# Performance work log

Hardware: AMD Instinct MI355X
Metric: run time of the kernel (lower is better)

Reference implementation:

```python
import jax, jax.numpy as jnp
import numpy as np
from jax import lax
from functools import partial

NPOINT = 2048
RADIUS = 1.0
NSAMPLE = 32


def _fps(xyz, npoint):
    # Farthest point sampling, sequential as in the classic CUDA kernel.
    # xyz: (N, 3) -> (npoint,) int32 indices; starts at index 0.
    N = xyz.shape[0]
    init_d = jnp.full((N,), jnp.inf, dtype=xyz.dtype)

    def step(carry, _):
        dists, last = carry
        delta = xyz - xyz[last]                      # (N, 3)
        nd = jnp.sum(delta * delta, axis=-1)         # (N,)
        dists = jnp.minimum(dists, nd)
        nxt = jnp.argmax(dists).astype(jnp.int32)
        return (dists, nxt), last

    (_, _), idxs = lax.scan(step, (init_d, jnp.int32(0)), None, length=npoint)
    return idxs


def _ball_query(radius, nsample, xyz, new_xyz):
    # xyz: (N, 3), new_xyz: (S, 3) -> (S, nsample) int32.
    # Take the first nsample points (in original order) within radius of each
    # centroid; pad with the first found index (centroid itself always hits).
    N = xyz.shape[0]
    d2 = (jnp.sum(new_xyz * new_xyz, -1, keepdims=True)
          + jnp.sum(xyz * xyz, -1)[None, :]
          - 2.0 * new_xyz @ xyz.T)                   # (S, N)
    mask = d2 < radius * radius
    key = jnp.where(mask, jnp.arange(N, dtype=jnp.int32), jnp.int32(N))  # (S, N)
    neg_topk, _ = lax.top_k(-key, nsample)           # nsample smallest keys
    idx = -neg_topk                                  # (S, nsample), ascending
    first = idx[:, :1]
    return jnp.where(idx == N, first, idx)


def setup_inputs() -> dict:
    key = jax.random.key(0)
    inputs = jax.random.normal(key, (4, 8192, 16), dtype=jnp.float32)
    return {"inputs": inputs}


def reference(inputs):
    xyz = inputs[..., :3]                            # (B, N, 3)
    points = inputs[..., 3:]                         # (B, N, C)

    fps_idx = jax.vmap(lambda p: _fps(p, NPOINT))(xyz)          # (B, S)
    new_xyz = jnp.take_along_axis(xyz, fps_idx[..., None], axis=1)  # (B, S, 3)

    idx = jax.vmap(partial(_ball_query, RADIUS, NSAMPLE))(xyz, new_xyz)  # (B, S, K)

    gather = jax.vmap(lambda p, i: p[i])             # (N, C), (S, K) -> (S, K, C)
    grouped_xyz = gather(xyz, idx) - new_xyz[:, :, None, :]      # (B, S, K, 3)
    grouped_points = gather(points, idx)                         # (B, S, K, C)
    new_points = jnp.concatenate([grouped_xyz, grouped_points], axis=-1)
    return new_xyz, new_points, idx, grouped_xyz
```

## Files before the change

### kernel.cpp

```cpp
#include <hip/hip_runtime.h>

#define NPOINT 2048
#define NSAMPLE 32
#define NPTS 8192
#define NB 4
#define CH 16
#define FPS_THREADS 1024
#define PTS_PER_THREAD (NPTS / FPS_THREADS)
#define FPS_WAVES (FPS_THREADS / 64)

typedef unsigned long long u64;

#define OFF_NEWXYZ 0
#define OFF_NEWPTS (NB * NPOINT * 3)
#define OFF_IDX (OFF_NEWPTS + NB * NPOINT * NSAMPLE * CH)
#define OFF_GXYZ (OFF_IDX + NB * NPOINT * NSAMPLE)

template <int CTRL>
__device__ __forceinline__ u64 dpp_max_round(u64 key) {
  unsigned lo = (unsigned)key, hi = (unsigned)(key >> 32);
  unsigned plo =
      (unsigned)__builtin_amdgcn_update_dpp(0, (int)lo, CTRL, 0xf, 0xf, true);
  unsigned phi =
      (unsigned)__builtin_amdgcn_update_dpp(0, (int)hi, CTRL, 0xf, 0xf, true);
  u64 other = ((u64)phi << 32) | plo;
  return other > key ? other : key;
}

__global__ __launch_bounds__(FPS_THREADS) void fps_kernel(
    const float* __restrict__ in, float* __restrict__ out) {
  __shared__ float4 lpxyz[NPTS];
  __shared__ float newb[NPOINT * 3];
  __shared__ u64 slots[2][FPS_WAVES];

  const int b = blockIdx.x;
  const int tid = threadIdx.x;
  const int lane = tid & 63;
  const int wv = tid >> 6;
  const float* base = in + (size_t)b * NPTS * CH;

  float px[PTS_PER_THREAD], py[PTS_PER_THREAD], pz[PTS_PER_THREAD],
      d[PTS_PER_THREAD];
#pragma unroll
  for (int j = 0; j < PTS_PER_THREAD; ++j) {
    int p = tid + j * FPS_THREADS;
    float4 r = *reinterpret_cast<const float4*>(base + (size_t)p * CH);
    px[j] = r.x;
    py[j] = r.y;
    pz[j] = r.z;
    lpxyz[p] = r;
    d[j] = __builtin_inff();
  }
  if (tid < FPS_WAVES)
    slots[0][tid] = (tid == 0) ? (((u64)0x7f800000u << 32) | 8191u) : 0ull;

  for (int it = 0; it < NPOINT; ++it) {
    const int pb = it & 1;
    __syncthreads();
    u64 k = slots[pb][lane & 15];
    k = dpp_max_round<0x111>(k);
    k = dpp_max_round<0x112>(k);
    k = dpp_max_round<0x114>(k);
    k = dpp_max_round<0x118>(k);
    const int gi =
        8191 -
        (int)(unsigned)__builtin_amdgcn_readlane((int)(unsigned)k, 15);
    float4 g = lpxyz[gi];
    const float gx = g.x, gy = g.y, gz = g.z;
    if (tid == 0) {
      newb[it * 3 + 0] = gx;
      newb[it * 3 + 1] = gy;
      newb[it * 3 + 2] = gz;
    }
    float bestv = -1.0f;
    int bestj = 0;
#pragma unroll
    for (int j = 0; j < PTS_PER_THREAD; ++j) {
      float dx = __fsub_rn(px[j], gx);
      float dy = __fsub_rn(py[j], gy);
      float dz = __fsub_rn(pz[j], gz);
      float nd = __fadd_rn(__fadd_rn(__fmul_rn(dx, dx), __fmul_rn(dy, dy)),
                           __fmul_rn(dz, dz));
      float dn = fminf(d[j], nd);
      d[j] = dn;
      if (dn > bestv) {
        bestv = dn;
        bestj = j;
      }
    }
    const int besti = tid + bestj * FPS_THREADS;
    u64 bestkey = ((u64)__float_as_uint(bestv) << 32) | (8191u - (unsigned)besti);
    bestkey = dpp_max_round<0x111>(bestkey);
    bestkey = dpp_max_round<0x112>(bestkey);
    bestkey = dpp_max_round<0x114>(bestkey);
    bestkey = dpp_max_round<0x118>(bestkey);
    bestkey = dpp_max_round<0x142>(bestkey);
    bestkey = dpp_max_round<0x143>(bestkey);
    if (lane == 63) slots[pb ^ 1][wv] = bestkey;
  }
  __syncthreads();
  float* ob = out + OFF_NEWXYZ + (size_t)b * NPOINT * 3;
  for (int i = tid; i < NPOINT * 3; i += FPS_THREADS) ob[i] = newb[i];
}

__device__ __forceinline__ void write_slot(float* __restrict__ out,
                                           const float* __restrict__ base,
                                           int b, int qi, int s, int p,
                                           float4 r0, float qx, float qy,
                                           float qz) {
  float dx = __fsub_rn(r0.x, qx);
  float dy = __fsub_rn(r0.y, qy);
  float dz = __fsub_rn(r0.z, qz);
  size_t qs = (size_t)b * NPOINT + qi;
  out[OFF_IDX + qs * NSAMPLE + s] = (float)p;
  float* g = out + OFF_GXYZ + (qs * NSAMPLE + s) * 3;
  g[0] = dx;
  g[1] = dy;
  g[2] = dz;
  const float* row = base + (size_t)p * CH;
  float4 r1 = *reinterpret_cast<const float4*>(row + 4);
  float4 r2 = *reinterpret_cast<const float4*>(row + 8);
  float4 r3 = *reinterpret_cast<const float4*>(row + 12);
  float* np_ = out + OFF_NEWPTS + (qs * NSAMPLE + s) * CH;
  *reinterpret_cast<float4*>(np_ + 0) = make_float4(dx, dy, dz, r0.w);
  *reinterpret_cast<float4*>(np_ + 4) = r1;
  *reinterpret_cast<float4*>(np_ + 8) = r2;
  *reinterpret_cast<float4*>(np_ + 12) = r3;
}

__global__ __launch_bounds__(256) void ballq_kernel(
    const float* __restrict__ in, float* __restrict__ out) {
  const int lane = threadIdx.x & 63;
  const int qid = blockIdx.x * 4 + (threadIdx.x >> 6);
  const int b = qid >> 11;
  const int qi = qid & 2047;
  const float* base = in + (size_t)b * NPTS * CH;
  const float* q = out + OFF_NEWXYZ + ((size_t)b * NPOINT + qi) * 3;
  float qx = q[0], qy = q[1], qz = q[2];
  float qn = __fadd_rn(__fadd_rn(__fmul_rn(qx, qx), __fmul_rn(qy, qy)),
                       __fmul_rn(qz, qz));

  int cnt = 0;
  int first = 0;
  bool have_first = false;
  for (int chunk = 0; chunk < NPTS / 64 && cnt < NSAMPLE; ++chunk) {
    int p = chunk * 64 + lane;
    float4 r0 = *reinterpret_cast<const float4*>(base + (size_t)p * CH);
    float pn =
        __fadd_rn(__fadd_rn(__fmul_rn(r0.x, r0.x), __fmul_rn(r0.y, r0.y)),
                  __fmul_rn(r0.z, r0.z));
    float dot =
        __fadd_rn(__fadd_rn(__fmul_rn(qx, r0.x), __fmul_rn(qy, r0.y)),
                  __fmul_rn(qz, r0.z));
    float d2 = __fsub_rn(__fadd_rn(qn, pn), __fmul_rn(2.0f, dot));
    bool in_r = d2 < 1.0f;
    unsigned long long mask = __ballot(in_r);
    if (!have_first && mask) {
      first = chunk * 64 + __builtin_ctzll(mask);
      have_first = true;
    }
    int pos = cnt + __popcll(mask & ((1ull << lane) - 1ull));
    if (in_r && pos < NSAMPLE) write_slot(out, base, b, qi, pos, p, r0, qx, qy, qz);
    cnt += __popcll(mask);
  }
  if (cnt < NSAMPLE) {
    int s = cnt + lane;
    if (s < NSAMPLE) {
      float4 r0 = *reinterpret_cast<const float4*>(base + (size_t)first * CH);
      write_slot(out, base, b, qi, s, first, r0, qx, qy, qz);
    }
  }
}

extern "C" void kernel_launch(void* const* d_in, const int* in_sizes, int n_in,
                              void* d_out, int out_size, void* d_ws,
                              size_t ws_size, hipStream_t stream) {
  (void)in_sizes;
  (void)n_in;
  (void)out_size;
  (void)d_ws;
  (void)ws_size;
  const float* in = (const float*)d_in[0];
  float* out = (float*)d_out;
  fps_kernel<<<NB, FPS_THREADS, 0, stream>>>(in, out);
  ballq_kernel<<<(NB * NPOINT) / 4, 256, 0, stream>>>(in, out);
}
```

Measured before the change: 2.167 ms.

## Use float-only DPP max with ballot tie-break and packed v2f FPS math

The FPS argmax reduction used to run DPP max rounds on packed 64-bit (distance, index) keys. It now reduces only the 32-bit float distance with DPP, then finds the winning lane with a ballot and readlane. This roughly halves the DPP traffic per round. Points are now assigned to threads contiguously, so each thread's point indices are consecutive. That keeps the lowest-index tie-break intact when combined with the ctz of the ballot. The distance math uses 2-wide float vectors so it can map to packed FP32 instructions, with fp contraction turned off to keep rounding exact.

```diff
diff --git a/kernel.cpp b/kernel.cpp
--- a/kernel.cpp
+++ b/kernel.cpp
@@ -1,4 +1,6 @@
 #include <hip/hip_runtime.h>
+
+#pragma clang fp contract(off)
 
 #define NPOINT 2048
 #define NSAMPLE 32
@@ -7,9 +9,11 @@
 #define CH 16
 #define FPS_THREADS 1024
 #define PTS_PER_THREAD (NPTS / FPS_THREADS)
+#define PAIRS (PTS_PER_THREAD / 2)
 #define FPS_WAVES (FPS_THREADS / 64)
 
 typedef unsigned long long u64;
+typedef float v2f __attribute__((ext_vector_type(2)));
 
 #define OFF_NEWXYZ 0
 #define OFF_NEWPTS (NB * NPOINT * 3)
@@ -17,14 +21,9 @@
 #define OFF_GXYZ (OFF_IDX + NB * NPOINT * NSAMPLE)
 
 template <int CTRL>
-__device__ __forceinline__ u64 dpp_max_round(u64 key) {
-  unsigned lo = (unsigned)key, hi = (unsigned)(key >> 32);
-  unsigned plo =
-      (unsigned)__builtin_amdgcn_update_dpp(0, (int)lo, CTRL, 0xf, 0xf, true);
-  unsigned phi =
-      (unsigned)__builtin_amdgcn_update_dpp(0, (int)hi, CTRL, 0xf, 0xf, true);
-  u64 other = ((u64)phi << 32) | plo;
-  return other > key ? other : key;
+__device__ __forceinline__ float dpp_fmax(float v) {
+  int o = __builtin_amdgcn_update_dpp(0, __float_as_int(v), CTRL, 0xf, 0xf, true);
+  return fmaxf(v, __int_as_float(o));
 }
 
 __global__ __launch_bounds__(FPS_THREADS) void fps_kernel(
@@ -39,32 +38,38 @@
   const int wv = tid >> 6;
   const float* base = in + (size_t)b * NPTS * CH;
 
-  float px[PTS_PER_THREAD], py[PTS_PER_THREAD], pz[PTS_PER_THREAD],
-      d[PTS_PER_THREAD];
+  v2f pxv[PAIRS], pyv[PAIRS], pzv[PAIRS], dv[PAIRS];
 #pragma unroll
-  for (int j = 0; j < PTS_PER_THREAD; ++j) {
-    int p = tid + j * FPS_THREADS;
-    float4 r = *reinterpret_cast<const float4*>(base + (size_t)p * CH);
-    px[j] = r.x;
-    py[j] = r.y;
-    pz[j] = r.z;
-    lpxyz[p] = r;
-    d[j] = __builtin_inff();
+  for (int jp = 0; jp < PAIRS; ++jp) {
+    int p0 = tid * PTS_PER_THREAD + 2 * jp;
+    float4 r0 = *reinterpret_cast<const float4*>(base + (size_t)p0 * CH);
+    float4 r1 = *reinterpret_cast<const float4*>(base + (size_t)(p0 + 1) * CH);
+    pxv[jp] = (v2f){r0.x, r1.x};
+    pyv[jp] = (v2f){r0.y, r1.y};
+    pzv[jp] = (v2f){r0.z, r1.z};
+    lpxyz[p0] = r0;
+    lpxyz[p0 + 1] = r1;
+    dv[jp] = (v2f){__builtin_inff(), __builtin_inff()};
   }
   if (tid < FPS_WAVES)
-    slots[0][tid] = (tid == 0) ? (((u64)0x7f800000u << 32) | 8191u) : 0ull;
+    slots[0][tid] = (tid == 0) ? (u64)0x7f800000u : (u64)0xbf800000u;
 
   for (int it = 0; it < NPOINT; ++it) {
     const int pb = it & 1;
     __syncthreads();
-    u64 k = slots[pb][lane & 15];
-    k = dpp_max_round<0x111>(k);
-    k = dpp_max_round<0x112>(k);
-    k = dpp_max_round<0x114>(k);
-    k = dpp_max_round<0x118>(k);
-    const int gi =
-        8191 -
-        (int)(unsigned)__builtin_amdgcn_readlane((int)(unsigned)k, 15);
+    u64 sl = slots[pb][lane & 15];
+    float sd = __int_as_float((int)(unsigned)sl);
+    int sidx = (int)(unsigned)(sl >> 32);
+    float m = sd;
+    m = dpp_fmax<0x111>(m);
+    m = dpp_fmax<0x112>(m);
+    m = dpp_fmax<0x114>(m);
+    m = dpp_fmax<0x118>(m);
+    const float smax =
+        __int_as_float(__builtin_amdgcn_readlane(__float_as_int(m), 15));
+    const u64 bal = __ballot(sd == smax) & 0xFFFFull;
+    const int wwin = (int)__builtin_ctzll(bal);
+    const int gi = __builtin_amdgcn_readlane(sidx, wwin);
     float4 g = lpxyz[gi];
     const float gx = g.x, gy = g.y, gz = g.z;
     if (tid == 0) {
@@ -73,30 +78,37 @@
       newb[it * 3 + 2] = gz;
     }
     float bestv = -1.0f;
+#pragma unroll
+    for (int jp = 0; jp < PAIRS; ++jp) {
+      v2f dx = pxv[jp] - gx;
+      v2f dy = pyv[jp] - gy;
+      v2f dz = pzv[jp] - gz;
+      v2f nd = (dx * dx + dy * dy) + dz * dz;
+      v2f dn = {fminf(dv[jp].x, nd.x), fminf(dv[jp].y, nd.y)};
+      dv[jp] = dn;
+      bestv = fmaxf(bestv, fmaxf(dn.x, dn.y));
+    }
+    const float* df = (const float*)dv;
     int bestj = 0;
 #pragma unroll
-    for (int j = 0; j < PTS_PER_THREAD; ++j) {
-      float dx = __fsub_rn(px[j], gx);
-      float dy = __fsub_rn(py[j], gy);
-      float dz = __fsub_rn(pz[j], gz);
-      float nd = __fadd_rn(__fadd_rn(__fmul_rn(dx, dx), __fmul_rn(dy, dy)),
-                           __fmul_rn(dz, dz));
-      float dn = fminf(d[j], nd);
-      d[j] = dn;
-      if (dn > bestv) {
-        bestv = dn;
-        bestj = j;
-      }
-    }
-    const int besti = tid + bestj * FPS_THREADS;
-    u64 bestkey = ((u64)__float_as_uint(bestv) << 32) | (8191u - (unsigned)besti);
-    bestkey = dpp_max_round<0x111>(bestkey);
-    bestkey = dpp_max_round<0x112>(bestkey);
-    bestkey = dpp_max_round<0x114>(bestkey);
-    bestkey = dpp_max_round<0x118>(bestkey);
-    bestkey = dpp_max_round<0x142>(bestkey);
-    bestkey = dpp_max_round<0x143>(bestkey);
-    if (lane == 63) slots[pb ^ 1][wv] = bestkey;
+    for (int jj = PTS_PER_THREAD - 1; jj >= 0; --jj)
+      if (df[jj] == bestv) bestj = jj;
+    const int besti = tid * PTS_PER_THREAD + bestj;
+    float wm = bestv;
+    wm = dpp_fmax<0x111>(wm);
+    wm = dpp_fmax<0x112>(wm);
+    wm = dpp_fmax<0x114>(wm);
+    wm = dpp_fmax<0x118>(wm);
+    wm = dpp_fmax<0x142>(wm);
+    wm = dpp_fmax<0x143>(wm);
+    const float swm =
+        __int_as_float(__builtin_amdgcn_readlane(__float_as_int(wm), 63));
+    const u64 wbal = __ballot(bestv == swm);
+    const int wl = (int)__builtin_ctzll(wbal);
+    const int widx = __builtin_amdgcn_readlane(besti, wl);
+    if (lane == 0)
+      slots[pb ^ 1][wv] =
+          ((u64)(unsigned)widx << 32) | (unsigned)__float_as_int(swm);
   }
   __syncthreads();
   float* ob = out + OFF_NEWXYZ + (size_t)b * NPOINT * 3;
```

Measured after the change: 2.029 ms. 6.4% less time.
